# Performance work log

Measured on AMD Instinct MI355X. Metric: run time of the kernel, lower is better.

The kernel has to match this reference:

```python
import jax, jax.numpy as jnp
import numpy as np

N = 100000
E = 1600000
D_IN = 128
F = 128


def _glorot(key, shape, scale=1.0):
    fan_in, fan_out = shape
    std = jnp.sqrt(2.0 / (fan_in + fan_out))
    return jax.random.normal(key, shape, dtype=jnp.float32) * std * scale


def setup_inputs() -> dict:
    key = jax.random.key(0)
    ks = jax.random.split(key, 10)
    h = jax.random.normal(ks[0], (N, D_IN), dtype=jnp.float32)
    # ensure every node appears as a row (src) so degree >= 1 (no inf in deg**-0.5)
    src_extra = jax.random.randint(ks[1], (E - N,), 0, N, dtype=jnp.int32)
    edge_src = jnp.concatenate([jnp.arange(N, dtype=jnp.int32), src_extra])
    edge_dst = jax.random.randint(ks[2], (E,), 0, N, dtype=jnp.int32)
    # faithful to original: fake indices sampled in [0, E) (jnp indexing clamps)
    src_fake = jax.random.randint(ks[3], (E,), 0, E, dtype=jnp.int32)
    dst_fake = jax.random.randint(ks[4], (E,), 0, E, dtype=jnp.int32)
    w_gcn0 = _glorot(ks[5], (D_IN, F))
    w_gcn1 = _glorot(ks[6], (F, F))
    # small scale on rate0 head to keep exp(sum over F dims) finite in fp32
    w_rate0 = _glorot(ks[7], (F, F), scale=0.05)
    w_rate1 = _glorot(ks[8], (F, 1))
    w_alpha = _glorot(ks[9], (F, 1))
    return {"h": h, "w_gcn0": w_gcn0, "w_gcn1": w_gcn1, "w_rate0": w_rate0,
            "w_rate1": w_rate1, "w_alpha": w_alpha, "edge_src": edge_src,
            "edge_dst": edge_dst, "src_fake": src_fake, "dst_fake": dst_fake}


def _gcn(h, W, norm, edge_src, edge_dst):
    h = h * norm                     # [N, d] degree pre-norm
    h = h @ W                        # dense projection
    h = jax.ops.segment_sum(h[edge_dst], edge_src, num_segments=N)  # a @ h
    return h * norm                  # degree post-norm


def reference(h, w_gcn0, w_gcn1, w_rate0, w_rate1, w_alpha,
              edge_src, edge_dst, src_fake, dst_fake):
    ones = jnp.ones((E,), dtype=h.dtype)
    deg = jax.ops.segment_sum(ones, edge_src, num_segments=N)  # row sums of a
    norm = (deg ** -0.5)[:, None]

    h = _gcn(h, w_gcn0, norm, edge_src, edge_dst)
    h = _gcn(h, w_gcn1, norm, edge_src, edge_dst)

    rate0 = h @ w_rate0   # [N, F]
    rate1 = h @ w_rate1   # [N, 1]
    alpha = h @ w_alpha   # [N, 1]

    src, dst = edge_src, edge_dst
    rate0_real = jnp.exp((rate0[src] + rate0[dst]).sum(-1))
    rate1_real = jnp.exp((rate1[src] + rate1[dst]).sum(-1))
    alpha_real = jax.nn.sigmoid((alpha[src] * alpha[dst]).sum(-1) / alpha.shape[-1] ** 0.5)

    # faithful to original (including rate0+rate1 mix and /shape (not sqrt) in alpha_fake)
    rate0_fake = jnp.exp((rate0[src_fake] + rate1[dst_fake]).sum(-1))
    rate1_fake = jnp.exp((rate1[src_fake] + rate1[dst_fake]).sum(-1))
    alpha_fake = jax.nn.sigmoid((alpha[src] * alpha[dst_fake]).sum(-1) / alpha.shape[-1])

    return jnp.stack([rate0_real, rate1_real, alpha_real,
                      rate0_fake, rate1_fake, alpha_fake])  # [6, E]
```

## Files before the change

kernel.cpp:

```cpp
#include <hip/hip_runtime.h>
#include <math.h>

#define NN 100000
#define EE 1600000
#define KB 256
#define RR 391
#define CAP 8192
#define NPART 391


__global__ __launch_bounds__(256) void k_init(int* __restrict__ gcur) {
    gcur[threadIdx.x] = 0;
}


__global__ __launch_bounds__(512) void k_part_proj(const int* __restrict__ src, const int* __restrict__ dst,
                                                   int* __restrict__ gcur, unsigned int* __restrict__ pk,
                                                   const float* __restrict__ h,
                                                   const float* __restrict__ w_gcn0,
                                                   const float* __restrict__ w_gcn1,
                                                   const float* __restrict__ w_rate0,
                                                   const float* __restrict__ w_rate1,
                                                   const float* __restrict__ w_alpha,
                                                   float4* __restrict__ u4) {
    __shared__ int cnt[KB];
    __shared__ int base[KB];
    __shared__ float V0[128], V1[128], V2[128];
    __shared__ float Q0[128], Q1[128], Q2[128];
    __shared__ alignas(16) float sP0[128], sP1[128], sP2[128];
    int t = threadIdx.x;
    int role = blockIdx.x & 1;
    int id = blockIdx.x >> 1;

    if (role == 0) {
        if (t < KB) cnt[t] = 0;
        __syncthreads();
        int e0 = id * 4096 + t * 8;
        unsigned int pkv[8];
        int bkt[8];
        if (e0 + 8 <= EE) {
            int4 sa = *(const int4*)(src + e0);
            int4 sb = *(const int4*)(src + e0 + 4);
            int4 da = *(const int4*)(dst + e0);
            int4 db = *(const int4*)(dst + e0 + 4);
            int ss[8] = { sa.x, sa.y, sa.z, sa.w, sb.x, sb.y, sb.z, sb.w };
            int dd[8] = { da.x, da.y, da.z, da.w, db.x, db.y, db.z, db.w };
            #pragma unroll
            for (int i = 0; i < 8; ++i) {
                int b = ss[i] / RR;
                bkt[i] = b;
                pkv[i] = (unsigned int)dd[i] | ((unsigned int)(ss[i] - b * RR) << 17);
                atomicAdd(&cnt[b], 1);
            }
        } else {
            #pragma unroll
            for (int i = 0; i < 8; ++i) {
                int e = e0 + i;
                if (e < EE) {
                    int s = src[e], d = dst[e];
                    int b = s / RR;
                    bkt[i] = b;
                    pkv[i] = (unsigned int)d | ((unsigned int)(s - b * RR) << 17);
                    atomicAdd(&cnt[b], 1);
                } else bkt[i] = -1;
            }
        }
        __syncthreads();
        if (t < KB) base[t] = cnt[t] ? atomicAdd(&gcur[t], cnt[t]) : 0;
        __syncthreads();
        if (t < KB) cnt[t] = 0;
        __syncthreads();
        #pragma unroll
        for (int i = 0; i < 8; ++i) {
            if (bkt[i] >= 0) {
                int rr = atomicAdd(&cnt[bkt[i]], 1);
                int rel = base[bkt[i]] + rr;
                if (rel < CAP) pk[bkt[i] * CAP + rel] = pkv[i];
            }
        }
    } else {
        int r = t >> 2, seg = t & 3;
        {
            const float4* pp = (const float4*)(w_rate0 + r * 128 + seg * 32);
            float s = 0.f;
            #pragma unroll
            for (int k = 0; k < 8; ++k) { float4 v = pp[k]; s += v.x + v.y + v.z + v.w; }
            s += __shfl_down(s, 2, 4); s += __shfl_down(s, 1, 4);
            if (seg == 0) V0[r] = s;
        }
        if (t < 128) { V1[t] = w_rate1[t]; V2[t] = w_alpha[t]; }
        __syncthreads();
        {
            const float4* pp = (const float4*)(w_gcn1 + r * 128 + seg * 32);
            float q0 = 0.f, q1 = 0.f, q2 = 0.f;
            #pragma unroll
            for (int k = 0; k < 8; ++k) {
                float4 w = pp[k];
                int j = seg * 32 + k * 4;
                q0 += w.x * V0[j] + w.y * V0[j+1] + w.z * V0[j+2] + w.w * V0[j+3];
                q1 += w.x * V1[j] + w.y * V1[j+1] + w.z * V1[j+2] + w.w * V1[j+3];
                q2 += w.x * V2[j] + w.y * V2[j+1] + w.z * V2[j+2] + w.w * V2[j+3];
            }
            q0 += __shfl_down(q0, 2, 4); q0 += __shfl_down(q0, 1, 4);
            q1 += __shfl_down(q1, 2, 4); q1 += __shfl_down(q1, 1, 4);
            q2 += __shfl_down(q2, 2, 4); q2 += __shfl_down(q2, 1, 4);
            if (seg == 0) { Q0[r] = q0; Q1[r] = q1; Q2[r] = q2; }
        }
        __syncthreads();
        {
            const float4* pp = (const float4*)(w_gcn0 + r * 128 + seg * 32);
            float q0 = 0.f, q1 = 0.f, q2 = 0.f;
            #pragma unroll
            for (int k = 0; k < 8; ++k) {
                float4 w = pp[k];
                int j = seg * 32 + k * 4;
                q0 += w.x * Q0[j] + w.y * Q0[j+1] + w.z * Q0[j+2] + w.w * Q0[j+3];
                q1 += w.x * Q1[j] + w.y * Q1[j+1] + w.z * Q1[j+2] + w.w * Q1[j+3];
                q2 += w.x * Q2[j] + w.y * Q2[j+1] + w.z * Q2[j+2] + w.w * Q2[j+3];
            }
            q0 += __shfl_down(q0, 2, 4); q0 += __shfl_down(q0, 1, 4);
            q1 += __shfl_down(q1, 2, 4); q1 += __shfl_down(q1, 1, 4);
            q2 += __shfl_down(q2, 2, 4); q2 += __shfl_down(q2, 1, 4);
            if (seg == 0) { sP0[r] = q0; sP1[r] = q1; sP2[r] = q2; }
        }
        __syncthreads();
        int hw = t >> 5;
        int l32 = t & 31;
        int c4 = l32 * 4;
        float4 c0 = *(const float4*)(sP0 + c4);
        float4 c1 = *(const float4*)(sP1 + c4);
        float4 c2 = *(const float4*)(sP2 + c4);
        int nlo = id * 256;
        for (int i0 = 0; i0 < 256; i0 += 16) {
            int node = nlo + i0 + hw;
            if (node < NN) {
                float4 hv = *(const float4*)(h + (size_t)node * 128 + c4);
                float p0v = hv.x * c0.x + hv.y * c0.y + hv.z * c0.z + hv.w * c0.w;
                float p1v = hv.x * c1.x + hv.y * c1.y + hv.z * c1.z + hv.w * c1.w;
                float p2v = hv.x * c2.x + hv.y * c2.y + hv.z * c2.z + hv.w * c2.w;
                #pragma unroll
                for (int off = 16; off > 0; off >>= 1) {
                    p0v += __shfl_down(p0v, off, 32);
                    p1v += __shfl_down(p1v, off, 32);
                    p2v += __shfl_down(p2v, off, 32);
                }
                if (l32 == 0) {
                    float* up = (float*)&u4[node];
                    *(float2*)up = make_float2(p0v, p1v);
                    up[2] = p2v;
                }
            }
        }
    }
}


__global__ __launch_bounds__(1024) void k_cnt(const unsigned int* __restrict__ pk,
                                              const int* __restrict__ gcur,
                                              float* __restrict__ nrm, float4* __restrict__ u4) {
    __shared__ int c[RR];
    int b = blockIdx.x;
    int t = threadIdx.x;
    int nlo = b * RR;
    int nn = NN - nlo; if (nn > RR) nn = RR;
    if (nn <= 0) return;
    if (t < RR) c[t] = 0;
    __syncthreads();
    const unsigned int* P = pk + b * CAP;
    int m = gcur[b]; if (m > CAP) m = CAP;
    for (int i = t; i < m; i += 1024) atomicAdd(&c[P[i] >> 17], 1);
    __syncthreads();
    if (t < nn) {
        float nv = rsqrtf((float)c[t]);
        nrm[nlo + t] = nv;
        ((float*)&u4[nlo + t])[3] = nv;
    }
}


template<int MODE>
__global__ __launch_bounds__(1024) void k_agg(const unsigned int* __restrict__ pk,
                                              const int* __restrict__ gcur,
                                              const float4* __restrict__ T, const float* __restrict__ nrm,
                                              float4* __restrict__ outv) {
    __shared__ float s0[RR], s1[RR], s2[RR];
    int b = blockIdx.x;
    int t = threadIdx.x;
    int nlo = b * RR;
    int nn = NN - nlo; if (nn > RR) nn = RR;
    if (nn <= 0) return;
    if (t < RR) { s0[t] = 0.f; s1[t] = 0.f; s2[t] = 0.f; }
    __syncthreads();
    const unsigned int* P = pk + b * CAP;
    int m = gcur[b]; if (m > CAP) m = CAP;
    int i = t;
    for (; i + 3072 < m; i += 4096) {
        unsigned int w0 = P[i];
        unsigned int w1 = P[i + 1024];
        unsigned int w2 = P[i + 2048];
        unsigned int w3 = P[i + 3072];
        float4 v0 = T[w0 & 0x1FFFFu];
        float4 v1 = T[w1 & 0x1FFFFu];
        float4 v2 = T[w2 & 0x1FFFFu];
        float4 v3 = T[w3 & 0x1FFFFu];
        if (MODE == 1) {
            v0.x *= v0.w; v0.y *= v0.w; v0.z *= v0.w;
            v1.x *= v1.w; v1.y *= v1.w; v1.z *= v1.w;
            v2.x *= v2.w; v2.y *= v2.w; v2.z *= v2.w;
            v3.x *= v3.w; v3.y *= v3.w; v3.z *= v3.w;
        }
        int r0 = (int)(w0 >> 17), r1 = (int)(w1 >> 17), r2 = (int)(w2 >> 17), r3 = (int)(w3 >> 17);
        atomicAdd(&s0[r0], v0.x); atomicAdd(&s1[r0], v0.y); atomicAdd(&s2[r0], v0.z);
        atomicAdd(&s0[r1], v1.x); atomicAdd(&s1[r1], v1.y); atomicAdd(&s2[r1], v1.z);
        atomicAdd(&s0[r2], v2.x); atomicAdd(&s1[r2], v2.y); atomicAdd(&s2[r2], v2.z);
        atomicAdd(&s0[r3], v3.x); atomicAdd(&s1[r3], v3.y); atomicAdd(&s2[r3], v3.z);
    }
    for (; i < m; i += 1024) {
        unsigned int wa = P[i];
        float4 va = T[wa & 0x1FFFFu];
        float ax = va.x, ay = va.y, az = va.z;
        if (MODE == 1) { ax *= va.w; ay *= va.w; az *= va.w; }
        int ra = (int)(wa >> 17);
        atomicAdd(&s0[ra], ax); atomicAdd(&s1[ra], ay); atomicAdd(&s2[ra], az);
    }
    __syncthreads();
    for (int j = t; j < nn; j += 1024) {
        float nv = nrm[nlo + j];
        float sc = (MODE == 1) ? nv * nv : nv;
        outv[nlo + j] = make_float4(sc * s0[j], sc * s1[j], sc * s2[j], 0.f);
    }
}


__global__ __launch_bounds__(256) void k_edge(const int* __restrict__ esrc, const int* __restrict__ edst,
                                              const int* __restrict__ sfake, const int* __restrict__ dfake,
                                              const float4* __restrict__ p4, float* __restrict__ out) {
    int t = threadIdx.x;
    int e0 = blockIdx.x * 1024 + t * 4;
    if (e0 >= EE) return;
    int4 s4  = *(const int4*)(esrc + e0);
    int4 d4  = *(const int4*)(edst + e0);
    int4 sf4 = *(const int4*)(sfake + e0);
    int4 df4 = *(const int4*)(dfake + e0);
    int ss[4] = { s4.x, s4.y, s4.z, s4.w };
    int dd[4] = { d4.x, d4.y, d4.z, d4.w };
    int sf[4] = { sf4.x, sf4.y, sf4.z, sf4.w };
    int df[4] = { df4.x, df4.y, df4.z, df4.w };
    float o0[4], o1[4], o2[4], o3[4], o4[4], o5[4];
    #pragma unroll
    for (int j = 0; j < 4; ++j) {
        int sfj = sf[j]; sfj = sfj < 0 ? 0 : (sfj >= NN ? NN - 1 : sfj);
        int dfj = df[j]; dfj = dfj < 0 ? 0 : (dfj >= NN ? NN - 1 : dfj);
        float4 ps = p4[ss[j]], pd = p4[dd[j]], psf = p4[sfj], pdf = p4[dfj];
        o0[j] = expf(ps.x + pd.x);
        o1[j] = expf(ps.y + pd.y);
        o2[j] = 1.f / (1.f + expf(-(ps.z * pd.z)));
        o3[j] = expf(psf.x + 128.f * pdf.y);
        o4[j] = expf(psf.y + pdf.y);
        o5[j] = 1.f / (1.f + expf(-(ps.z * pdf.z)));
    }
    *(float4*)(out + e0)                  = make_float4(o0[0], o0[1], o0[2], o0[3]);
    *(float4*)(out + (size_t)EE + e0)     = make_float4(o1[0], o1[1], o1[2], o1[3]);
    *(float4*)(out + (size_t)2 * EE + e0) = make_float4(o2[0], o2[1], o2[2], o2[3]);
    *(float4*)(out + (size_t)3 * EE + e0) = make_float4(o3[0], o3[1], o3[2], o3[3]);
    *(float4*)(out + (size_t)4 * EE + e0) = make_float4(o4[0], o4[1], o4[2], o4[3]);
    *(float4*)(out + (size_t)5 * EE + e0) = make_float4(o5[0], o5[1], o5[2], o5[3]);
}


extern "C" void kernel_launch(void* const* d_in, const int* in_sizes, int n_in,
                              void* d_out, int out_size, void* d_ws, size_t ws_size,
                              hipStream_t stream) {
    const float* h       = (const float*)d_in[0];
    const float* w_gcn0  = (const float*)d_in[1];
    const float* w_gcn1  = (const float*)d_in[2];
    const float* w_rate0 = (const float*)d_in[3];
    const float* w_rate1 = (const float*)d_in[4];
    const float* w_alpha = (const float*)d_in[5];
    const int* edge_src  = (const int*)d_in[6];
    const int* edge_dst  = (const int*)d_in[7];
    const int* src_fake  = (const int*)d_in[8];
    const int* dst_fake  = (const int*)d_in[9];
    float* out = (float*)d_out;

    char* p = (char*)d_ws;
    auto alloc = [&](size_t bytes) {
        char* r = p;
        p += (bytes + 255) & ~(size_t)255;
        return r;
    };
    unsigned int* pk = (unsigned int*)alloc((size_t)KB * CAP * 4);
    int* gcur   = (int*)alloc(KB * 4);
    float* nrm  = (float*)alloc((size_t)NN * 4);
    float4* u4  = (float4*)alloc((size_t)NN * 16);
    float4* z4  = (float4*)alloc((size_t)NN * 16);
    float4* p4  = (float4*)alloc((size_t)NN * 16);

    k_init<<<1, KB, 0, stream>>>(gcur);
    k_part_proj<<<2 * NPART, 512, 0, stream>>>(edge_src, edge_dst, gcur, pk, h,
                                               w_gcn0, w_gcn1, w_rate0, w_rate1, w_alpha, u4);
    k_cnt<<<KB, 1024, 0, stream>>>(pk, gcur, nrm, u4);
    k_agg<1><<<KB, 1024, 0, stream>>>(pk, gcur, u4, nrm, z4);
    k_agg<2><<<KB, 1024, 0, stream>>>(pk, gcur, z4, nrm, p4);
    k_edge<<<(EE + 1023) / 1024, 256, 0, stream>>>(edge_src, edge_dst, src_fake, dst_fake, p4, out);
}
```

Measured before the change: 247.0 us.

## Hoist weight-product precompute into init kernel, reuse atomic ranks, unroll projection

Measured after the change: 225.7 us. -8.6%, faster.

```diff
diff --git a/kernel.cpp b/kernel.cpp
--- a/kernel.cpp
+++ b/kernel.cpp
@@ -9,24 +9,66 @@
 #define NPART 391
 
 
-__global__ __launch_bounds__(256) void k_init(int* __restrict__ gcur) {
-    gcur[threadIdx.x] = 0;
+__global__ __launch_bounds__(1024) void k_pmat(const float* __restrict__ w_gcn0,
+                                               const float* __restrict__ w_gcn1,
+                                               const float* __restrict__ w_rate0,
+                                               const float* __restrict__ w_rate1,
+                                               const float* __restrict__ w_alpha,
+                                               float* __restrict__ Pt0, float* __restrict__ Pt1,
+                                               float* __restrict__ Pt2, int* __restrict__ gcur) {
+    __shared__ float V0[128], V1[128], V2[128];
+    __shared__ float Q0[128], Q1[128], Q2[128];
+    int t = threadIdx.x;
+    if (t < KB) gcur[t] = 0;
+    int r = t >> 3, seg = t & 7;
+    {
+        const float* p = w_rate0 + r * 128 + seg * 16;
+        float s = 0.f;
+        #pragma unroll
+        for (int k = 0; k < 16; ++k) s += p[k];
+        s += __shfl_down(s, 4, 8); s += __shfl_down(s, 2, 8); s += __shfl_down(s, 1, 8);
+        if (seg == 0) V0[r] = s;
+    }
+    if (t < 128) { V1[t] = w_rate1[t]; V2[t] = w_alpha[t]; }
+    __syncthreads();
+    {
+        const float* p = w_gcn1 + r * 128 + seg * 16;
+        float q0 = 0.f, q1 = 0.f, q2 = 0.f;
+        #pragma unroll
+        for (int k = 0; k < 16; ++k) {
+            float w = p[k]; int j = seg * 16 + k;
+            q0 += w * V0[j]; q1 += w * V1[j]; q2 += w * V2[j];
+        }
+        q0 += __shfl_down(q0, 4, 8); q0 += __shfl_down(q0, 2, 8); q0 += __shfl_down(q0, 1, 8);
+        q1 += __shfl_down(q1, 4, 8); q1 += __shfl_down(q1, 2, 8); q1 += __shfl_down(q1, 1, 8);
+        q2 += __shfl_down(q2, 4, 8); q2 += __shfl_down(q2, 2, 8); q2 += __shfl_down(q2, 1, 8);
+        if (seg == 0) { Q0[r] = q0; Q1[r] = q1; Q2[r] = q2; }
+    }
+    __syncthreads();
+    {
+        const float* p = w_gcn0 + r * 128 + seg * 16;
+        float q0 = 0.f, q1 = 0.f, q2 = 0.f;
+        #pragma unroll
+        for (int k = 0; k < 16; ++k) {
+            float w = p[k]; int j = seg * 16 + k;
+            q0 += w * Q0[j]; q1 += w * Q1[j]; q2 += w * Q2[j];
+        }
+        q0 += __shfl_down(q0, 4, 8); q0 += __shfl_down(q0, 2, 8); q0 += __shfl_down(q0, 1, 8);
+        q1 += __shfl_down(q1, 4, 8); q1 += __shfl_down(q1, 2, 8); q1 += __shfl_down(q1, 1, 8);
+        q2 += __shfl_down(q2, 4, 8); q2 += __shfl_down(q2, 2, 8); q2 += __shfl_down(q2, 1, 8);
+        if (seg == 0) { Pt0[r] = q0; Pt1[r] = q1; Pt2[r] = q2; }
+    }
 }
 
 
 __global__ __launch_bounds__(512) void k_part_proj(const int* __restrict__ src, const int* __restrict__ dst,
                                                    int* __restrict__ gcur, unsigned int* __restrict__ pk,
                                                    const float* __restrict__ h,
-                                                   const float* __restrict__ w_gcn0,
-                                                   const float* __restrict__ w_gcn1,
-                                                   const float* __restrict__ w_rate0,
-                                                   const float* __restrict__ w_rate1,
-                                                   const float* __restrict__ w_alpha,
+                                                   const float* __restrict__ Pt0, const float* __restrict__ Pt1,
+                                                   const float* __restrict__ Pt2,
                                                    float4* __restrict__ u4) {
     __shared__ int cnt[KB];
     __shared__ int base[KB];
-    __shared__ float V0[128], V1[128], V2[128];
-    __shared__ float Q0[128], Q1[128], Q2[128];
     __shared__ alignas(16) float sP0[128], sP1[128], sP2[128];
     int t = threadIdx.x;
     int role = blockIdx.x & 1;
@@ -37,7 +79,7 @@
         __syncthreads();
         int e0 = id * 4096 + t * 8;
         unsigned int pkv[8];
-        int bkt[8];
+        int bkt[8], rnk[8];
         if (e0 + 8 <= EE) {
             int4 sa = *(const int4*)(src + e0);
             int4 sb = *(const int4*)(src + e0 + 4);
@@ -50,7 +92,7 @@
                 int b = ss[i] / RR;
                 bkt[i] = b;
                 pkv[i] = (unsigned int)dd[i] | ((unsigned int)(ss[i] - b * RR) << 17);
-                atomicAdd(&cnt[b], 1);
+                rnk[i] = atomicAdd(&cnt[b], 1);
             }
         } else {
             #pragma unroll
@@ -61,68 +103,22 @@
                     int b = s / RR;
                     bkt[i] = b;
                     pkv[i] = (unsigned int)d | ((unsigned int)(s - b * RR) << 17);
-                    atomicAdd(&cnt[b], 1);
+                    rnk[i] = atomicAdd(&cnt[b], 1);
                 } else bkt[i] = -1;
             }
         }
         __syncthreads();
         if (t < KB) base[t] = cnt[t] ? atomicAdd(&gcur[t], cnt[t]) : 0;
-        __syncthreads();
-        if (t < KB) cnt[t] = 0;
         __syncthreads();
         #pragma unroll
         for (int i = 0; i < 8; ++i) {
             if (bkt[i] >= 0) {
-                int rr = atomicAdd(&cnt[bkt[i]], 1);
-                int rel = base[bkt[i]] + rr;
+                int rel = base[bkt[i]] + rnk[i];
                 if (rel < CAP) pk[bkt[i] * CAP + rel] = pkv[i];
             }
         }
     } else {
-        int r = t >> 2, seg = t & 3;
-        {
-            const float4* pp = (const float4*)(w_rate0 + r * 128 + seg * 32);
-            float s = 0.f;
-            #pragma unroll
-            for (int k = 0; k < 8; ++k) { float4 v = pp[k]; s += v.x + v.y + v.z + v.w; }
-            s += __shfl_down(s, 2, 4); s += __shfl_down(s, 1, 4);
-            if (seg == 0) V0[r] = s;
-        }
-        if (t < 128) { V1[t] = w_rate1[t]; V2[t] = w_alpha[t]; }
-        __syncthreads();
-        {
-            const float4* pp = (const float4*)(w_gcn1 + r * 128 + seg * 32);
-            float q0 = 0.f, q1 = 0.f, q2 = 0.f;
-            #pragma unroll
-            for (int k = 0; k < 8; ++k) {
-                float4 w = pp[k];
-                int j = seg * 32 + k * 4;
-                q0 += w.x * V0[j] + w.y * V0[j+1] + w.z * V0[j+2] + w.w * V0[j+3];
-                q1 += w.x * V1[j] + w.y * V1[j+1] + w.z * V1[j+2] + w.w * V1[j+3];
-                q2 += w.x * V2[j] + w.y * V2[j+1] + w.z * V2[j+2] + w.w * V2[j+3];
-            }
-            q0 += __shfl_down(q0, 2, 4); q0 += __shfl_down(q0, 1, 4);
-            q1 += __shfl_down(q1, 2, 4); q1 += __shfl_down(q1, 1, 4);
-            q2 += __shfl_down(q2, 2, 4); q2 += __shfl_down(q2, 1, 4);
-            if (seg == 0) { Q0[r] = q0; Q1[r] = q1; Q2[r] = q2; }
-        }
-        __syncthreads();
-        {
-            const float4* pp = (const float4*)(w_gcn0 + r * 128 + seg * 32);
-            float q0 = 0.f, q1 = 0.f, q2 = 0.f;
-            #pragma unroll
-            for (int k = 0; k < 8; ++k) {
-                float4 w = pp[k];
-                int j = seg * 32 + k * 4;
-                q0 += w.x * Q0[j] + w.y * Q0[j+1] + w.z * Q0[j+2] + w.w * Q0[j+3];
-                q1 += w.x * Q1[j] + w.y * Q1[j+1] + w.z * Q1[j+2] + w.w * Q1[j+3];
-                q2 += w.x * Q2[j] + w.y * Q2[j+1] + w.z * Q2[j+2] + w.w * Q2[j+3];
-            }
-            q0 += __shfl_down(q0, 2, 4); q0 += __shfl_down(q0, 1, 4);
-            q1 += __shfl_down(q1, 2, 4); q1 += __shfl_down(q1, 1, 4);
-            q2 += __shfl_down(q2, 2, 4); q2 += __shfl_down(q2, 1, 4);
-            if (seg == 0) { sP0[r] = q0; sP1[r] = q1; sP2[r] = q2; }
-        }
+        if (t < 128) { sP0[t] = Pt0[t]; sP1[t] = Pt1[t]; sP2[t] = Pt2[t]; }
         __syncthreads();
         int hw = t >> 5;
         int l32 = t & 31;
@@ -131,23 +127,37 @@
         float4 c1 = *(const float4*)(sP1 + c4);
         float4 c2 = *(const float4*)(sP2 + c4);
         int nlo = id * 256;
-        for (int i0 = 0; i0 < 256; i0 += 16) {
-            int node = nlo + i0 + hw;
-            if (node < NN) {
-                float4 hv = *(const float4*)(h + (size_t)node * 128 + c4);
-                float p0v = hv.x * c0.x + hv.y * c0.y + hv.z * c0.z + hv.w * c0.w;
-                float p1v = hv.x * c1.x + hv.y * c1.y + hv.z * c1.z + hv.w * c1.w;
-                float p2v = hv.x * c2.x + hv.y * c2.y + hv.z * c2.z + hv.w * c2.w;
-                #pragma unroll
-                for (int off = 16; off > 0; off >>= 1) {
-                    p0v += __shfl_down(p0v, off, 32);
-                    p1v += __shfl_down(p1v, off, 32);
-                    p2v += __shfl_down(p2v, off, 32);
+        for (int i0 = 0; i0 < 256; i0 += 32) {
+            int nodeA = nlo + i0 + hw;
+            int nodeB = nodeA + 16;
+            bool vA = nodeA < NN, vB = nodeB < NN;
+            float4 ha = vA ? *(const float4*)(h + (size_t)nodeA * 128 + c4) : make_float4(0.f,0.f,0.f,0.f);
+            float4 hb = vB ? *(const float4*)(h + (size_t)nodeB * 128 + c4) : make_float4(0.f,0.f,0.f,0.f);
+            float a0 = ha.x * c0.x + ha.y * c0.y + ha.z * c0.z + ha.w * c0.w;
+            float a1 = ha.x * c1.x + ha.y * c1.y + ha.z * c1.z + ha.w * c1.w;
+            float a2 = ha.x * c2.x + ha.y * c2.y + ha.z * c2.z + ha.w * c2.w;
+            float b0 = hb.x * c0.x + hb.y * c0.y + hb.z * c0.z + hb.w * c0.w;
+            float b1 = hb.x * c1.x + hb.y * c1.y + hb.z * c1.z + hb.w * c1.w;
+            float b2 = hb.x * c2.x + hb.y * c2.y + hb.z * c2.z + hb.w * c2.w;
+            #pragma unroll
+            for (int off = 16; off > 0; off >>= 1) {
+                a0 += __shfl_down(a0, off, 32);
+                a1 += __shfl_down(a1, off, 32);
+                a2 += __shfl_down(a2, off, 32);
+                b0 += __shfl_down(b0, off, 32);
+                b1 += __shfl_down(b1, off, 32);
+                b2 += __shfl_down(b2, off, 32);
+            }
+            if (l32 == 0) {
+                if (vA) {
+                    float* up = (float*)&u4[nodeA];
+                    *(float2*)up = make_float2(a0, a1);
+                    up[2] = a2;
                 }
-                if (l32 == 0) {
-                    float* up = (float*)&u4[node];
-                    *(float2*)up = make_float2(p0v, p1v);
-                    up[2] = p2v;
+                if (vB) {
+                    float* up = (float*)&u4[nodeB];
+                    *(float2*)up = make_float2(b0, b1);
+                    up[2] = b2;
                 }
             }
         }
@@ -295,10 +305,14 @@
     float4* u4  = (float4*)alloc((size_t)NN * 16);
     float4* z4  = (float4*)alloc((size_t)NN * 16);
     float4* p4  = (float4*)alloc((size_t)NN * 16);
-
-    k_init<<<1, KB, 0, stream>>>(gcur);
+    float* Pt0  = (float*)alloc(512);
+    float* Pt1  = (float*)alloc(512);
+    float* Pt2  = (float*)alloc(512);
+
+    k_pmat<<<1, 1024, 0, stream>>>(w_gcn0, w_gcn1, w_rate0, w_rate1, w_alpha,
+                                   Pt0, Pt1, Pt2, gcur);
     k_part_proj<<<2 * NPART, 512, 0, stream>>>(edge_src, edge_dst, gcur, pk, h,
-                                               w_gcn0, w_gcn1, w_rate0, w_rate1, w_alpha, u4);
+                                               Pt0, Pt1, Pt2, u4);
     k_cnt<<<KB, 1024, 0, stream>>>(pk, gcur, nrm, u4);
     k_agg<1><<<KB, 1024, 0, stream>>>(pk, gcur, u4, nrm, z4);
     k_agg<2><<<KB, 1024, 0, stream>>>(pk, gcur, z4, nrm, p4);
```
